# Optimization experiments

Measured on AMD Instinct MI355X. Metric: run time of the kernel, lower is better.

The kernel has to match this reference:

```python
import jax, jax.numpy as jnp
import numpy as np
import math
from jax import lax

KPAD = 4  # padding for 9x9 depthwise conv (same spatial size)

def dwconv(x, w, b):
    # x: [B,C,H,W], w: [C,1,9,9] depthwise (groups=C), b: [C]
    y = lax.conv_general_dilated(
        x, w, window_strides=(1, 1), padding=[(KPAD, KPAD), (KPAD, KPAD)],
        dimension_numbers=("NCHW", "OIHW", "NCHW"), feature_group_count=x.shape[1])
    return y + b[None, :, None, None]

def channel_pos_encoding(c, h, w, dtype):
    # position over channels, frequencies over the flattened spatial dim
    hw = h * w
    position = jnp.arange(c, dtype=jnp.float32)[:, None]                  # [C,1]
    div_term = jnp.exp(jnp.arange(0, hw, 2, dtype=jnp.float32) * (-math.log(10000.0) / hw))  # [hw/2]
    ang = position * div_term                                             # [C,hw/2]
    pe = jnp.stack([jnp.sin(ang), jnp.cos(ang)], axis=-1).reshape(c, hw)  # interleave sin/cos
    return pe.reshape(c, h, w).astype(dtype)

def setup_inputs() -> dict:
    key = jax.random.key(0)
    ks = jax.random.split(key, 9)
    B, C, H, W = 4, 256, 128, 128
    x = jax.random.normal(ks[0], (B, C, H, W), dtype=jnp.float32)
    def wgt(k):
        return jax.random.normal(k, (C, 1, 9, 9), dtype=jnp.float32) * 0.1
    return {
        "x": x,
        "q_w": wgt(ks[1]), "q_b": jax.random.normal(ks[2], (C,), dtype=jnp.float32) * 0.1,
        "k_w": wgt(ks[3]), "k_b": jax.random.normal(ks[4], (C,), dtype=jnp.float32) * 0.1,
        "v_w": wgt(ks[5]), "v_b": jax.random.normal(ks[6], (C,), dtype=jnp.float32) * 0.1,
        "o_w": wgt(ks[7]), "o_b": jax.random.normal(ks[8], (C,), dtype=jnp.float32) * 0.1,
        "num_heads": 8,
    }

def reference(x, q_w, q_b, k_w, k_b, v_w, v_b, o_w, o_b, num_heads):
    b, c, h, w = x.shape
    hw = h * w
    d = hw // num_heads  # per-head spatial dim
    x = x + channel_pos_encoding(c, h, w, x.dtype)[None]
    q = dwconv(x, q_w, q_b).reshape(b, c, num_heads, d)  # [B,C,H,D]
    k = dwconv(x, k_w, k_b).reshape(b, c, num_heads, d)
    v = dwconv(x, v_w, v_b).reshape(b, c, num_heads, d)
    # channel-over-channel attention in fp32 (matches forced fp32 cast)
    qk = jnp.einsum("bqhd,bkhd->bhqk", q.astype(jnp.float32), k.astype(jnp.float32)) / math.sqrt(hw)
    attn = jax.nn.softmax(qk, axis=-1)
    a = jnp.einsum("bhqk,bkhd->bqhd", attn.astype(v.dtype), v).reshape(b, c, h, w)
    return dwconv(a, o_w, o_b)
```

## Files before the change

kernel.cpp:

```cpp
#include <hip/hip_runtime.h>
#include <hip/hip_bf16.h>
#include <math.h>

#define BB 4
#define CC 256
#define HH 128
#define WW 128
#define HWS (HH*WW)
#define NHEADS 8
#define DD (HWS/NHEADS)

typedef __attribute__((ext_vector_type(8))) short bf16x8;
typedef __attribute__((ext_vector_type(4))) float f32x4;
typedef __attribute__((ext_vector_type(2))) __fp16 h16x2;
typedef __attribute__((ext_vector_type(8))) __fp16 h16x8;

#define GLD_LDS(g, l) __builtin_amdgcn_global_load_lds( \
    (const __attribute__((address_space(1))) void*)(g),  \
    (__attribute__((address_space(3))) void*)(l), 16, 0, 0)

static __device__ __forceinline__ unsigned short f2bf(float f) {
    unsigned int u = __float_as_uint(f);
    unsigned int r = (u + 0x7FFFu + ((u >> 16) & 1u)) >> 16;
    return (unsigned short)r;
}
static __device__ __forceinline__ float b2f(unsigned short u) {
    return __uint_as_float((unsigned int)u << 16);
}
static __device__ __forceinline__ unsigned int pk2(float a, float b) {
    union { h16x2 h; unsigned int u; } x;
    x.h = __builtin_amdgcn_cvt_pkrtz(a, b);
    return x.u;
}

__global__ __launch_bounds__(256) void build_wt(
    const float* __restrict__ qw, const float* __restrict__ kw,
    const float* __restrict__ vw, unsigned short* __restrict__ wt)
{
    const int c = blockIdx.x, cv = blockIdx.y;
    const float* w = (cv == 0) ? qw : (cv == 1) ? kw : vw;
    unsigned short* dst = wt + ((size_t)c * 3 + cv) * 9 * 512;
    for (int idx = threadIdx.x; idx < 9 * 512; idx += 256) {
        const int ky   = idx >> 9;
        const int rem  = idx & 511;
        const int lane = rem >> 3, e = rem & 7;
        const int m = lane & 15;
        const int k = ((lane >> 4) << 3) + e;
        const int d = k - m;
        const float v = (d >= 0 && d <= 8) ? w[c * 81 + ky * 9 + d] : 0.0f;
        const __fp16 hv = (__fp16)v;
        unsigned short bits;
        __builtin_memcpy(&bits, &hv, 2);
        dst[idx] = bits;
    }
}

#define FOFF 27648
#define PE_COEF   (-1.1243088e-3f)
#define PE_RSTEP  (0.99887632f)
__global__ __launch_bounds__(512, 6) void conv9qkv(
    const float* __restrict__ in,
    const unsigned short* __restrict__ wt,
    const float* __restrict__ b0, const float* __restrict__ b1,
    const float* __restrict__ b2,
    unsigned short* __restrict__ o0, unsigned short* __restrict__ o1,
    unsigned short* __restrict__ o2)
{
    __shared__ alignas(16) char lds[FOFF + 21760];

    const int u    = ((blockIdx.x & 7) << 8) + (blockIdx.x >> 3);
    const int c    = u >> 3;
    const int bidx = (u >> 1) & 3;
    const int tc   = (u & 1) << 6;
    const int tid  = threadIdx.x;
    const int lane = tid & 63;
    const int wr   = tid >> 6;
    const int r16  = lane & 15;
    const int g    = lane >> 4;

    for (int f = wr; f < 27; f += 8) {
        const char* src = (const char*)wt + (((size_t)c * 27 + f) << 10) + (lane << 4);
        GLD_LDS(src, lds + (f << 10) + (lane << 4));
    }

    const float* xp = in + ((size_t)(bidx * CC + c) << 14);
    const float cf  = (float)c;

    #pragma unroll
    for (int it = 0; it < 3; ++it) {
        const int i = tid + (it << 9);
        if (i < 1360) {
            const int row = i / 10;
            const int c8  = i - row * 10;
            const int gy  = row - 4;
            const int gx  = tc + (c8 << 3) - 4;
            uint4 wv = make_uint4(0u, 0u, 0u, 0u);
            if (gy >= 0 && gy < HH) {
                const float* xr = xp + (gy << 7);
                if (gx >= 0 && gx + 7 < WW) {
                    const float4 a0 = *(const float4*)(xr + gx);
                    const float4 a1 = *(const float4*)(xr + gx + 4);
                    float dt = __expf(PE_COEF * (float)(((gy << 7) + gx) >> 1));
                    float s, cc;
                    __sincosf(cf * dt, &s, &cc);
                    wv.x = pk2(a0.x + s, a0.y + cc);
                    dt *= PE_RSTEP;
                    __sincosf(cf * dt, &s, &cc);
                    wv.y = pk2(a0.z + s, a0.w + cc);
                    dt *= PE_RSTEP;
                    __sincosf(cf * dt, &s, &cc);
                    wv.z = pk2(a1.x + s, a1.y + cc);
                    dt *= PE_RSTEP;
                    __sincosf(cf * dt, &s, &cc);
                    wv.w = pk2(a1.z + s, a1.w + cc);
                } else {
                    float vv[8];
                    #pragma unroll
                    for (int e = 0; e < 8; ++e) {
                        const int gxe = gx + e;
                        float xv = 0.f;
                        if (gxe >= 0 && gxe < WW) {
                            const int flat = (gy << 7) + gxe;
                            const float dt = __expf(PE_COEF * (float)(flat >> 1));
                            float s, cc;
                            __sincosf(cf * dt, &s, &cc);
                            xv = xr[gxe] + ((flat & 1) ? cc : s);
                        }
                        vv[e] = xv;
                    }
                    wv.x = pk2(vv[0], vv[1]); wv.y = pk2(vv[2], vv[3]);
                    wv.z = pk2(vv[4], vv[5]); wv.w = pk2(vv[6], vv[7]);
                }
            }
            int byte = row * 160 + (c8 << 4);
            byte ^= (row & 7) << 4;
            *(uint4*)(lds + FOFF + byte) = wv;
        }
    }
    __syncthreads();

    f32x4 acc[3][4];
    {
        const float bq = b0[c], bk = b1[c], bv = b2[c];
        #pragma unroll
        for (int xt = 0; xt < 4; ++xt) {
            acc[0][xt] = (f32x4){bq, bq, bq, bq};
            acc[1][xt] = (f32x4){bk, bk, bk, bk};
            acc[2][xt] = (f32x4){bv, bv, bv, bv};
        }
    }

    const int rowbase = (wr << 4) + r16;
    __builtin_amdgcn_s_setprio(1);
    for (int ky = 0; ky < 9; ++ky) {
        const int row = rowbase + ky;
        const int sx  = (row & 7) << 4;
        const int rb  = row * 160 + (g << 4);
        h16x8 a[4];
        #pragma unroll
        for (int xt = 0; xt < 4; ++xt)
            a[xt] = *(const h16x8*)(lds + FOFF + ((rb + (xt << 5)) ^ sx));
        #pragma unroll
        for (int cv = 0; cv < 3; ++cv) {
            const h16x8 tf = *(const h16x8*)(lds + ((cv * 9 + ky) << 10) + (lane << 4));
            #pragma unroll
            for (int xt = 0; xt < 4; ++xt)
                acc[cv][xt] = __builtin_amdgcn_mfma_f32_16x16x32_f16(
                    tf, a[xt], acc[cv][xt], 0, 0, 0);
        }
    }
    __builtin_amdgcn_s_setprio(0);

    unsigned short* const outs[3] = { o0, o1, o2 };
    const size_t base = (((size_t)(bidx * NHEADS + wr) * CC + c) << 11)
                      + ((size_t)r16 << 7) + tc + (g << 2);
    #pragma unroll
    for (int cv = 0; cv < 3; ++cv)
        #pragma unroll
        for (int xt = 0; xt < 4; ++xt) {
            ushort4 uo;
            uo.x = f2bf(acc[cv][xt][0]); uo.y = f2bf(acc[cv][xt][1]);
            uo.z = f2bf(acc[cv][xt][2]); uo.w = f2bf(acc[cv][xt][3]);
            *(ushort4*)(outs[cv] + base + (xt << 4)) = uo;
        }
}

#define O_FRAG_OFF 11520
__global__ __launch_bounds__(256, 7) void conv9o(
    const unsigned short* __restrict__ ain,
    const float* __restrict__ w, const float* __restrict__ b,
    float* __restrict__ out)
{
    __shared__ alignas(16) char lds[O_FRAG_OFF + 9216];
    __shared__ float lw[81];

    const int u    = ((blockIdx.x & 7) << 9) + (blockIdx.x >> 3);
    const int c    = u >> 4;
    const int bidx = (u >> 2) & 3;
    const int t    = u & 3;
    const int plane = bidx * CC + c;
    const int tr   = (t >> 1) << 6;
    const int tc   = (t & 1) << 6;
    const int tid  = threadIdx.x;
    const int lane = tid & 63;
    const int wr   = tid >> 6;
    const int r16  = lane & 15;
    const int g    = lane >> 4;

    if (tid < 81) lw[tid] = w[c * 81 + tid];

    const unsigned short* ap = ain + (size_t)plane * HWS;

    #pragma unroll
    for (int it = 0; it < 3; ++it) {
        const int i = tid + (it << 8);
        if (i < 720) {
            const int row = i / 10;
            const int c8  = i - row * 10;
            const int gy  = tr + row - 4;
            const int gx  = tc + (c8 << 3) - 4;
            uint4 wv = make_uint4(0u, 0u, 0u, 0u);
            if (gy >= 0 && gy < HH) {
                const unsigned short* ar = ap + (gy << 7);
                if (gx >= 0 && gx + 7 < WW) {
                    const bf16x8 uu = *(const bf16x8*)(ar + gx);
                    wv.x = pk2(b2f((unsigned short)uu[0]), b2f((unsigned short)uu[1]));
                    wv.y = pk2(b2f((unsigned short)uu[2]), b2f((unsigned short)uu[3]));
                    wv.z = pk2(b2f((unsigned short)uu[4]), b2f((unsigned short)uu[5]));
                    wv.w = pk2(b2f((unsigned short)uu[6]), b2f((unsigned short)uu[7]));
                } else {
                    float vv[8];
                    #pragma unroll
                    for (int e = 0; e < 8; ++e) {
                        const int gxe = gx + e;
                        vv[e] = (gxe >= 0 && gxe < WW) ? b2f(ar[gxe]) : 0.f;
                    }
                    wv.x = pk2(vv[0], vv[1]); wv.y = pk2(vv[2], vv[3]);
                    wv.z = pk2(vv[4], vv[5]); wv.w = pk2(vv[6], vv[7]);
                }
            }
            int byte = row * 160 + (c8 << 4);
            byte ^= (row & 7) << 4;
            *(uint4*)(lds + byte) = wv;
        }
    }
    __syncthreads();

    {
        const int ln = tid >> 2, qq = tid & 3;
        const int m  = ln & 15;
        const int k0 = ((ln >> 4) << 3) + (qq << 1);
        const int d0 = k0 - m, d1 = k0 + 1 - m;
        #pragma unroll
        for (int ky = 0; ky < 9; ++ky) {
            const float f0 = (d0 >= 0 && d0 <= 8) ? lw[ky * 9 + d0] : 0.f;
            const float f1 = (d1 >= 0 && d1 <= 8) ? lw[ky * 9 + d1] : 0.f;
            *(unsigned int*)(lds + O_FRAG_OFF + (ky << 10) + (ln << 4) + (qq << 2)) = pk2(f0, f1);
        }
    }
    __syncthreads();

    const float bv = b[c];
    f32x4 acc[4];
    #pragma unroll
    for (int xt = 0; xt < 4; ++xt) acc[xt] = (f32x4){bv, bv, bv, bv};

    const int rowbase = (wr << 4) + r16;
    __builtin_amdgcn_s_setprio(1);
    for (int ky = 0; ky < 9; ++ky) {
        const int row = rowbase + ky;
        const int sx  = (row & 7) << 4;
        const int rb  = row * 160 + (g << 4);
        h16x8 a[4];
        #pragma unroll
        for (int xt = 0; xt < 4; ++xt)
            a[xt] = *(const h16x8*)(lds + ((rb + (xt << 5)) ^ sx));
        const h16x8 tf = *(const h16x8*)(lds + O_FRAG_OFF + (ky << 10) + (lane << 4));
        #pragma unroll
        for (int xt = 0; xt < 4; ++xt)
            acc[xt] = __builtin_amdgcn_mfma_f32_16x16x32_f16(tf, a[xt], acc[xt], 0, 0, 0);
    }
    __builtin_amdgcn_s_setprio(0);

    const int y = tr + (wr << 4) + r16;
    float* orow = out + (size_t)plane * HWS + (size_t)y * WW + tc + (g << 2);
    #pragma unroll
    for (int xt = 0; xt < 4; ++xt)
        *(f32x4*)(orow + (xt << 4)) = acc[xt];
}

template<bool IS_QK>
__global__ __launch_bounds__(256) void gemm_bf16(
    const unsigned short* __restrict__ Abuf, const unsigned short* __restrict__ Bbuf,
    void* __restrict__ Dout)
{
    constexpr int KT = 2048;

    __shared__ char lds[24576];

    const int tid = threadIdx.x;
    const int bh  = blockIdx.z;
    const int m0  = blockIdx.y << 7;
    const int n0  = blockIdx.x << 6;

    const unsigned short* Ab = Abuf + (size_t)bh * CC * KT + (size_t)m0 * KT;
    const unsigned short* Bb = Bbuf + (size_t)bh * CC * KT + (size_t)n0 * KT;

    const int lane = tid & 63;
    const int w    = tid >> 6;
    const int wm   = (w >> 1) << 6;
    const int wn   = (w & 1) << 5;
    const int r16  = lane & 15;
    const int g    = lane >> 4;

    const int trow = tid >> 3;
    const int slot = tid & 7;

    f32x4 acc[4][2] = {};

    for (int kt = 0; kt < KT / 64; ++kt) {
        const int kc = kt << 6;
        #pragma unroll
        for (int i = 0; i < 4; ++i) {
            const int row = (i << 5) + trow;
            const int gs  = slot ^ (row & 7);
            const char* srcp = (const char*)(Ab + (size_t)row * KT + kc) + gs * 16;
            GLD_LDS(srcp, lds + (i << 12) + tid * 16);
        }
        #pragma unroll
        for (int i = 0; i < 2; ++i) {
            const int row = (i << 5) + trow;
            const int gs  = slot ^ (row & 7);
            const char* srcp = (const char*)(Bb + (size_t)row * KT + kc) + gs * 16;
            GLD_LDS(srcp, lds + 16384 + (i << 12) + tid * 16);
        }
        __syncthreads();
        #pragma unroll
        for (int kk = 0; kk < 2; ++kk) {
            bf16x8 af[4], bfr[2];
            #pragma unroll
            for (int mi = 0; mi < 4; ++mi) {
                const int row = wm + (mi << 4) + r16;
                af[mi] = *(const bf16x8*)(lds + row * 128 + ((((kk << 2) + g) ^ (row & 7)) << 4));
            }
            #pragma unroll
            for (int nj = 0; nj < 2; ++nj) {
                const int row = wn + (nj << 4) + r16;
                bfr[nj] = *(const bf16x8*)(lds + 16384 + row * 128 + ((((kk << 2) + g) ^ (row & 7)) << 4));
            }
            #pragma unroll
            for (int mi = 0; mi < 4; ++mi)
                #pragma unroll
                for (int nj = 0; nj < 2; ++nj)
                    acc[mi][nj] = __builtin_amdgcn_mfma_f32_16x16x32_bf16(af[mi], bfr[nj], acc[mi][nj], 0, 0, 0);
        }
        __syncthreads();
    }

    float* sp = (float*)Dout + (size_t)bh * 65536;
    #pragma unroll
    for (int mi = 0; mi < 4; ++mi)
        #pragma unroll
        for (int nj = 0; nj < 2; ++nj)
            #pragma unroll
            for (int j = 0; j < 4; ++j) {
                const int row = m0 + wm + (mi << 4) + (g << 2) + j;
                const int col = n0 + wn + (nj << 4) + r16;
                sp[(size_t)row * 256 + col] = acc[mi][nj][j] * 0.0078125f;
            }
}

__global__ __launch_bounds__(256) void softmax_kernel(
    const float* __restrict__ S, unsigned short* __restrict__ P)
{
    const int row  = (blockIdx.x << 2) + (threadIdx.x >> 6);
    const int lane = threadIdx.x & 63;
    const float4 vv = *(const float4*)(S + ((size_t)row << 8) + (lane << 2));
    float m = fmaxf(fmaxf(vv.x, vv.y), fmaxf(vv.z, vv.w));
    #pragma unroll
    for (int o = 32; o; o >>= 1) m = fmaxf(m, __shfl_xor(m, o, 64));
    const float e0 = __expf(vv.x - m), e1 = __expf(vv.y - m);
    const float e2 = __expf(vv.z - m), e3 = __expf(vv.w - m);
    float s = (e0 + e1) + (e2 + e3);
    #pragma unroll
    for (int o = 32; o; o >>= 1) s += __shfl_xor(s, o, 64);
    const float r = 1.0f / s;
    ushort4 u;
    u.x = f2bf(e0 * r); u.y = f2bf(e1 * r); u.z = f2bf(e2 * r); u.w = f2bf(e3 * r);
    *(ushort4*)(P + ((size_t)row << 8) + (lane << 2)) = u;
}

__global__ __launch_bounds__(256) void gemm_pv(
    const unsigned short* __restrict__ Pbuf, const unsigned short* __restrict__ vbuf,
    unsigned short* __restrict__ Ao)
{
    __shared__ alignas(16) char lds[49152];

    const int tid = threadIdx.x;
    const int bh  = blockIdx.z;
    const int m0  = blockIdx.y << 7;
    const int n0  = blockIdx.x << 6;

    const unsigned short* Ab = Pbuf + ((size_t)bh << 16) + ((size_t)m0 << 8);

    const int lane = tid & 63;
    const int w    = tid >> 6;
    const int wm   = (w >> 1) << 6;
    const int wn   = (w & 1) << 5;
    const int r16  = lane & 15;
    const int g    = lane >> 4;
    const int trow = tid >> 3;
    const int slot = tid & 7;

    {
        #pragma unroll
        for (int i = 0; i < 4; ++i) {
            const int row = (i << 5) + trow;
            const int gs  = slot ^ (row & 7);
            GLD_LDS((const char*)(Ab + (size_t)row * 256) + gs * 16,
                    lds + (i << 12) + tid * 16);
        }
    }

    {
        const unsigned short* Vb = vbuf + (size_t)bh * (CC * DD) + n0;
        const int rl = tid >> 2, q4 = tid & 3;
        #pragma unroll
        for (int p = 0; p < 4; ++p) {
            const int cp = (p << 6) + rl;
            const unsigned short* src = Vb + (size_t)cp * DD + (q4 << 4);
            const bf16x8 v0 = *(const bf16x8*)(src);
            const bf16x8 v1 = *(const bf16x8*)(src + 8);
            const int cb = cp << 1;
            #pragma unroll
            for (int e = 0; e < 8; ++e) {
                const int d0 = (q4 << 4) + e, d1 = d0 + 8;
                *(unsigned short*)(lds + 16384 + d0 * 512 +
                    (cb ^ (((d0 & 7) ^ (d0 >> 3)) << 4))) = (unsigned short)v0[e];
                *(unsigned short*)(lds + 16384 + d1 * 512 +
                    (cb ^ (((d1 & 7) ^ (d1 >> 3)) << 4))) = (unsigned short)v1[e];
            }
        }
    }
    __syncthreads();

    f32x4 acc[4][2] = {};

    for (int kt = 0; kt < 4; ++kt) {
        #pragma unroll
        for (int kk = 0; kk < 2; ++kk) {
            bf16x8 af[4], bfr[2];
            #pragma unroll
            for (int mi = 0; mi < 4; ++mi) {
                const int row = wm + (mi << 4) + r16;
                af[mi] = *(const bf16x8*)(lds + row * 128 + ((((kk << 2) + g) ^ (row & 7)) << 4));
            }
            #pragma unroll
            for (int nj = 0; nj < 2; ++nj) {
                const int d = wn + (nj << 4) + r16;
                const int kbyte = (kt << 7) + ((((kk << 2) + g)) << 4);
                bfr[nj] = *(const bf16x8*)(lds + 16384 + d * 512 +
                    (kbyte ^ (((d & 7) ^ (d >> 3)) << 4)));
            }
            #pragma unroll
            for (int mi = 0; mi < 4; ++mi)
                #pragma unroll
                for (int nj = 0; nj < 2; ++nj)
                    acc[mi][nj] = __builtin_amdgcn_mfma_f32_16x16x32_bf16(af[mi], bfr[nj], acc[mi][nj], 0, 0, 0);
        }
        if (kt < 3) {
            __syncthreads();
            const int kc = (kt + 1) << 6;
            #pragma unroll
            for (int i = 0; i < 4; ++i) {
                const int row = (i << 5) + trow;
                const int gs  = slot ^ (row & 7);
                GLD_LDS((const char*)(Ab + (size_t)row * 256 + kc) + gs * 16,
                        lds + (i << 12) + tid * 16);
            }
            __syncthreads();
        }
    }

    const int b = bh >> 3, h = bh & 7;
    #pragma unroll
    for (int mi = 0; mi < 4; ++mi)
        #pragma unroll
        for (int nj = 0; nj < 2; ++nj)
            #pragma unroll
            for (int j = 0; j < 4; ++j) {
                const int row = m0 + wm + (mi << 4) + (g << 2) + j;
                const int col = n0 + wn + (nj << 4) + r16;
                Ao[((size_t)b * CC + row) * HWS + h * DD + col] = f2bf(acc[mi][nj][j]);
            }
}

extern "C" void kernel_launch(void* const* d_in, const int* in_sizes, int n_in,
                              void* d_out, int out_size, void* d_ws, size_t ws_size,
                              hipStream_t stream)
{
    const float* x  = (const float*)d_in[0];
    const float* qw = (const float*)d_in[1];
    const float* qb = (const float*)d_in[2];
    const float* kw = (const float*)d_in[3];
    const float* kb = (const float*)d_in[4];
    const float* vw = (const float*)d_in[5];
    const float* vb = (const float*)d_in[6];
    const float* ow = (const float*)d_in[7];
    const float* ob = (const float*)d_in[8];
    float* out = (float*)d_out;

    char* wsb = (char*)d_ws;
    __hip_bfloat16* q   = (__hip_bfloat16*)(wsb + 16777216UL);
    __hip_bfloat16* k   = (__hip_bfloat16*)(wsb + 50331648UL);
    float*          S   = (float*)(wsb + 83886080UL);
    __hip_bfloat16* P   = (__hip_bfloat16*)(wsb + 92274688UL);
    __hip_bfloat16* v   = (__hip_bfloat16*)(wsb + 96468992UL);
    unsigned short* A   = (unsigned short*)(wsb + 0);
    unsigned short* wt  = (unsigned short*)(wsb + 83886080UL);

    build_wt<<<dim3(CC, 3), 256, 0, stream>>>(qw, kw, vw, wt);
    conv9qkv<<<dim3(CC * 8), 512, 0, stream>>>(
        x, wt, qb, kb, vb,
        (unsigned short*)q, (unsigned short*)k, (unsigned short*)v);
    gemm_bf16<true><<<dim3(4, 2, 32), 256, 0, stream>>>(
        (const unsigned short*)q, (const unsigned short*)k, (void*)S);
    softmax_kernel<<<dim3(2048), 256, 0, stream>>>(S, (unsigned short*)P);
    gemm_pv<<<dim3(32, 2, 32), 256, 0, stream>>>(
        (const unsigned short*)P, (const unsigned short*)v, A);
    conv9o<<<dim3(BB * CC * 4), 256, 0, stream>>>(A, ow, ob, out);
}
```

Baseline: 150.4 us.

## Double-buffer QK GEMM loads and enlarge output conv tile to full height

The QK GEMM gets a two-stage LDS buffer, so the global-to-LDS loads for the next K tile are issued while MFMAs run on the current one. This is meant to hide load latency in a grid of only 256 blocks, at the cost of doubling its LDS footprint. The output depthwise conv now uses 512-thread blocks, each covering a 128x64 tile spanning the full plane height. That cuts the vertical halo re-reads per output and halves the block count, in exchange for more LDS per block and fewer, larger blocks.

```diff
diff --git a/kernel.cpp b/kernel.cpp
--- a/kernel.cpp
+++ b/kernel.cpp
@@ -185,22 +185,20 @@
         }
 }
 
-#define O_FRAG_OFF 11520
-__global__ __launch_bounds__(256, 7) void conv9o(
+#define OTILE 21760
+__global__ __launch_bounds__(512, 8) void conv9o(
     const unsigned short* __restrict__ ain,
     const float* __restrict__ w, const float* __restrict__ b,
     float* __restrict__ out)
 {
-    __shared__ alignas(16) char lds[O_FRAG_OFF + 9216];
+    __shared__ alignas(16) char lds[OTILE + 9216];
     __shared__ float lw[81];
 
-    const int u    = ((blockIdx.x & 7) << 9) + (blockIdx.x >> 3);
-    const int c    = u >> 4;
-    const int bidx = (u >> 2) & 3;
-    const int t    = u & 3;
+    const int u    = ((blockIdx.x & 7) << 8) + (blockIdx.x >> 3);
+    const int c    = u >> 3;
+    const int bidx = (u >> 1) & 3;
+    const int tc   = (u & 1) << 6;
     const int plane = bidx * CC + c;
-    const int tr   = (t >> 1) << 6;
-    const int tc   = (t & 1) << 6;
     const int tid  = threadIdx.x;
     const int lane = tid & 63;
     const int wr   = tid >> 6;
@@ -209,15 +207,15 @@
 
     if (tid < 81) lw[tid] = w[c * 81 + tid];
 
-    const unsigned short* ap = ain + (size_t)plane * HWS;
+    const unsigned short* ap = ain + ((size_t)plane << 14);
 
     #pragma unroll
     for (int it = 0; it < 3; ++it) {
-        const int i = tid + (it << 8);
-        if (i < 720) {
+        const int i = tid + (it << 9);
+        if (i < 1360) {
             const int row = i / 10;
             const int c8  = i - row * 10;
-            const int gy  = tr + row - 4;
+            const int gy  = row - 4;
             const int gx  = tc + (c8 << 3) - 4;
             uint4 wv = make_uint4(0u, 0u, 0u, 0u);
             if (gy >= 0 && gy < HH) {
@@ -246,7 +244,7 @@
     }
     __syncthreads();
 
-    {
+    if (tid < 256) {
         const int ln = tid >> 2, qq = tid & 3;
         const int m  = ln & 15;
         const int k0 = ((ln >> 4) << 3) + (qq << 1);
@@ -255,7 +253,7 @@
         for (int ky = 0; ky < 9; ++ky) {
             const float f0 = (d0 >= 0 && d0 <= 8) ? lw[ky * 9 + d0] : 0.f;
             const float f1 = (d1 >= 0 && d1 <= 8) ? lw[ky * 9 + d1] : 0.f;
-            *(unsigned int*)(lds + O_FRAG_OFF + (ky << 10) + (ln << 4) + (qq << 2)) = pk2(f0, f1);
+            *(unsigned int*)(lds + OTILE + (ky << 10) + (ln << 4) + (qq << 2)) = pk2(f0, f1);
         }
     }
     __syncthreads();
@@ -275,28 +273,27 @@
         #pragma unroll
         for (int xt = 0; xt < 4; ++xt)
             a[xt] = *(const h16x8*)(lds + ((rb + (xt << 5)) ^ sx));
-        const h16x8 tf = *(const h16x8*)(lds + O_FRAG_OFF + (ky << 10) + (lane << 4));
+        const h16x8 tf = *(const h16x8*)(lds + OTILE + (ky << 10) + (lane << 4));
         #pragma unroll
         for (int xt = 0; xt < 4; ++xt)
             acc[xt] = __builtin_amdgcn_mfma_f32_16x16x32_f16(tf, a[xt], acc[xt], 0, 0, 0);
     }
     __builtin_amdgcn_s_setprio(0);
 
-    const int y = tr + (wr << 4) + r16;
-    float* orow = out + (size_t)plane * HWS + (size_t)y * WW + tc + (g << 2);
+    const int y = (wr << 4) + r16;
+    float* orow = out + ((size_t)plane << 14) + ((size_t)y << 7) + tc + (g << 2);
     #pragma unroll
     for (int xt = 0; xt < 4; ++xt)
         *(f32x4*)(orow + (xt << 4)) = acc[xt];
 }
 
-template<bool IS_QK>
-__global__ __launch_bounds__(256) void gemm_bf16(
+__global__ __launch_bounds__(256) void gemm_qk(
     const unsigned short* __restrict__ Abuf, const unsigned short* __restrict__ Bbuf,
-    void* __restrict__ Dout)
+    float* __restrict__ Sout)
 {
     constexpr int KT = 2048;
 
-    __shared__ char lds[24576];
+    __shared__ char lds[49152];
 
     const int tid = threadIdx.x;
     const int bh  = blockIdx.z;
@@ -318,35 +315,44 @@
 
     f32x4 acc[4][2] = {};
 
-    for (int kt = 0; kt < KT / 64; ++kt) {
+    auto stage = [&](int h, int kt) {
         const int kc = kt << 6;
+        char* base = lds + h * 24576;
         #pragma unroll
         for (int i = 0; i < 4; ++i) {
             const int row = (i << 5) + trow;
             const int gs  = slot ^ (row & 7);
-            const char* srcp = (const char*)(Ab + (size_t)row * KT + kc) + gs * 16;
-            GLD_LDS(srcp, lds + (i << 12) + tid * 16);
+            GLD_LDS((const char*)(Ab + (size_t)row * KT + kc) + gs * 16,
+                    base + (i << 12) + tid * 16);
         }
         #pragma unroll
         for (int i = 0; i < 2; ++i) {
             const int row = (i << 5) + trow;
             const int gs  = slot ^ (row & 7);
-            const char* srcp = (const char*)(Bb + (size_t)row * KT + kc) + gs * 16;
-            GLD_LDS(srcp, lds + 16384 + (i << 12) + tid * 16);
-        }
-        __syncthreads();
+            GLD_LDS((const char*)(Bb + (size_t)row * KT + kc) + gs * 16,
+                    base + 16384 + (i << 12) + tid * 16);
+        }
+    };
+
+    stage(0, 0);
+    __syncthreads();
+
+    for (int kt = 0; kt < KT / 64; ++kt) {
+        const int cur = kt & 1;
+        if (kt + 1 < KT / 64) stage(cur ^ 1, kt + 1);
+        const char* hb = lds + cur * 24576;
         #pragma unroll
         for (int kk = 0; kk < 2; ++kk) {
             bf16x8 af[4], bfr[2];
             #pragma unroll
             for (int mi = 0; mi < 4; ++mi) {
                 const int row = wm + (mi << 4) + r16;
-                af[mi] = *(const bf16x8*)(lds + row * 128 + ((((kk << 2) + g) ^ (row & 7)) << 4));
+                af[mi] = *(const bf16x8*)(hb + row * 128 + ((((kk << 2) + g) ^ (row & 7)) << 4));
             }
             #pragma unroll
             for (int nj = 0; nj < 2; ++nj) {
                 const int row = wn + (nj << 4) + r16;
-                bfr[nj] = *(const bf16x8*)(lds + 16384 + row * 128 + ((((kk << 2) + g) ^ (row & 7)) << 4));
+                bfr[nj] = *(const bf16x8*)(hb + 16384 + row * 128 + ((((kk << 2) + g) ^ (row & 7)) << 4));
             }
             #pragma unroll
             for (int mi = 0; mi < 4; ++mi)
@@ -357,7 +363,7 @@
         __syncthreads();
     }
 
-    float* sp = (float*)Dout + (size_t)bh * 65536;
+    float* sp = Sout + (size_t)bh * 65536;
     #pragma unroll
     for (int mi = 0; mi < 4; ++mi)
         #pragma unroll
@@ -523,10 +529,10 @@
     conv9qkv<<<dim3(CC * 8), 512, 0, stream>>>(
         x, wt, qb, kb, vb,
         (unsigned short*)q, (unsigned short*)k, (unsigned short*)v);
-    gemm_bf16<true><<<dim3(4, 2, 32), 256, 0, stream>>>(
-        (const unsigned short*)q, (const unsigned short*)k, (void*)S);
+    gemm_qk<<<dim3(4, 2, 32), 256, 0, stream>>>(
+        (const unsigned short*)q, (const unsigned short*)k, S);
     softmax_kernel<<<dim3(2048), 256, 0, stream>>>(S, (unsigned short*)P);
     gemm_pv<<<dim3(32, 2, 32), 256, 0, stream>>>(
         (const unsigned short*)P, (const unsigned short*)v, A);
-    conv9o<<<dim3(BB * CC * 4), 256, 0, stream>>>(A, ow, ob, out);
-}
+    conv9o<<<dim3(CC * 8), 512, 0, stream>>>(A, ow, ob, out);
+}
```

New measurement: 143.1 us. -4.9%, faster.
